# Performance work log

Hardware: AMD Instinct MI355X
Metric: run time of the kernel (lower is better)

## Reference

```python
import jax, jax.numpy as jnp
import numpy as np

N = 8192
F_IN = 128
F_OUT = 64
ALPHA = 0.2
NEG_INF = -9.0e15  # matches -9000000000000000.0 in the torch source


def setup_inputs() -> dict:
    key = jax.random.key(0)
    k1, k2, k3, k4 = jax.random.split(key, 4)
    h = jax.random.normal(k1, (N, F_IN), dtype=jnp.float32)
    adj = jax.random.randint(k2, (N, N), 0, 2).astype(jnp.int32)
    W = jax.random.normal(k3, (F_IN, F_OUT), dtype=jnp.float32) * 0.05
    a = jax.random.normal(k4, (2 * F_OUT,), dtype=jnp.float32) * 0.05
    return {"h": h, "adj": adj, "W": W, "a": a}


def reference(h, adj, W, a):
    # Wh: [N, F_OUT]
    Wh = h @ W
    # a([Wh_i ; Wh_j]) == Wh_i @ a1 + Wh_j @ a2 -> avoid O(N^2*2F) concat
    a1, a2 = a[:F_OUT], a[F_OUT:]
    s_src = Wh @ a1  # [N] contribution of row node i
    s_dst = Wh @ a2  # [N] contribution of col node j
    e = jax.nn.leaky_relu(s_src[:, None] + s_dst[None, :], negative_slope=ALPHA)  # [N, N]
    e = jnp.where(adj > 0, e, NEG_INF)
    attention = jax.nn.softmax(e, axis=1)  # [N, N]
    h_prime = attention @ Wh  # [N, F_OUT]
    return jax.nn.elu(h_prime)
```

## Files before the change

### kernel.cpp

```cpp
#include <hip/hip_runtime.h>
#include <hip/hip_bf16.h>

#define N 8192
#define FIN 128
#define FOUT 64
#define CSPLIT 2
#define CHUNK (N / CSPLIT)
#define M 32
#define TILE 128
#define NT (CHUNK / TILE)
#define LOG2E 1.44269504f

typedef __attribute__((ext_vector_type(4))) float f32x4;
typedef __attribute__((ext_vector_type(4))) int i32x4;
typedef __attribute__((ext_vector_type(8))) short bf16x8;

#define GLOAD_LDS16(gp, lp)                                                    \
    __builtin_amdgcn_global_load_lds(                                          \
        (const __attribute__((address_space(1))) void*)(gp),                   \
        (__attribute__((address_space(3))) void*)(lp), 16, 0, 0)

__global__ __launch_bounds__(256) void wh_kernel(
    const float* __restrict__ h, const float* __restrict__ W,
    const float* __restrict__ a,
    __hip_bfloat16* __restrict__ whT, float* __restrict__ s_src,
    float* __restrict__ s_dst) {
    __shared__ float Wl[FIN * FOUT];
    const int w = threadIdx.x >> 6;
    const int lane = threadIdx.x & 63;
#pragma unroll
    for (int q = 0; q < 8; ++q) {
        const int i = w * 8 + q;
        GLOAD_LDS16(W + i * 256 + lane * 4, &Wl[i * 256]);
    }
    asm volatile("s_waitcnt vmcnt(0)" ::: "memory");
    __syncthreads();

    const int row = blockIdx.x * 4 + w;
    const float* hr = h + (size_t)row * FIN;
    float acc = 0.f;
#pragma unroll
    for (int k0 = 0; k0 < FIN; k0 += 4) {
        f32x4 hv = *(const f32x4*)(hr + k0);
        acc += hv[0] * Wl[(k0 + 0) * FOUT + lane];
        acc += hv[1] * Wl[(k0 + 1) * FOUT + lane];
        acc += hv[2] * Wl[(k0 + 2) * FOUT + lane];
        acc += hv[3] * Wl[(k0 + 3) * FOUT + lane];
    }
    whT[(size_t)lane * N + row] = __float2bfloat16(acc);
    float s1 = acc * a[lane];
    float s2 = acc * a[FOUT + lane];
#pragma unroll
    for (int mm = 32; mm >= 1; mm >>= 1) {
        s1 += __shfl_xor(s1, mm, 64);
        s2 += __shfl_xor(s2, mm, 64);
    }
    if (lane == 0) { s_src[row] = s1 * LOG2E; s_dst[row] = s2 * LOG2E; }
}

__global__ __launch_bounds__(512, 4) void gat_partial(
    const int* __restrict__ adj, const __hip_bfloat16* __restrict__ whT,
    const float* __restrict__ s_src, const float* __restrict__ s_dst,
    float* __restrict__ numP, float* __restrict__ denP) {
    union SMem {
        struct {
            int adjb[2][M][TILE];
            short whb[2][FOUT][TILE];
            float sdl[CHUNK];
        } s;
        struct { float pC[4][M][FOUT]; float pD[4][M]; } e;
    };
    __shared__ SMem sm;

    const int tid = threadIdx.x;
    const int w = tid >> 6, lane = tid & 63;
    const int m = lane & 15, kg = lane >> 4;
    const int wr = w >> 2, wc = w & 3;
    const int rg = blockIdx.x >> 1;
    const int c = blockIdx.x & 1;
    const int ibase = rg * M;
    const int cb = c * CHUNK;
    const int aRow = wr * 16 + m;
    const float ssrc = s_src[ibase + aRow];
    const int sidx = w * 2;

    f32x4 acc[4] = {{0,0,0,0},{0,0,0,0},{0,0,0,0},{0,0,0,0}};
    f32x4 acc4 = {0,0,0,0};
    const short oneb = (m == 0) ? (short)0x3F80 : (short)0;
    const bf16x8 bones = {oneb, oneb, oneb, oneb, oneb, oneb, oneb, oneb};

    auto stage = [&](int t, int buf) {
        const int gcol = cb + t * TILE;
#pragma unroll
        for (int q = 0; q < 2; ++q) {
            const int idx = sidx + q;
            const int r = idx * 2 + (lane >> 5);
            const int b = ((lane & 31) * 16) ^ ((r & 31) << 4);
            GLOAD_LDS16(adj + (size_t)(ibase + r) * N + gcol + (b >> 2),
                        &sm.s.adjb[buf][idx * 2][0]);
        }
#pragma unroll
        for (int q = 0; q < 2; ++q) {
            const int idx = sidx + q;
            const int f = idx * 4 + (lane >> 4);
            const int b = ((lane & 15) * 16) ^ ((f & 15) << 4);
            GLOAD_LDS16(whT + (size_t)f * N + gcol + (b >> 1),
                        &sm.s.whb[buf][idx * 4][0]);
        }
    };

#pragma unroll
    for (int q = 0; q < 2; ++q) {
        const int idx = sidx + q;
        GLOAD_LDS16(s_dst + cb + idx * 256 + lane * 4, &sm.s.sdl[idx * 256]);
    }
    stage(0, 0);
    stage(1, 1);
    asm volatile("s_waitcnt vmcnt(4)" ::: "memory");
    __builtin_amdgcn_s_barrier();

#pragma unroll 2
    for (int t = 0; t < NT; ++t) {
        const int buf = t & 1;

        {
            const int kcol = wc * 32 + kg * 8;
            const char* adjbase = (const char*)&sm.s.adjb[buf][0][0];
            const int aswz = (aRow & 31) << 4;
            i32x4 a0 = *(const i32x4*)(adjbase + aRow * 512 + ((kcol * 4) ^ aswz));
            i32x4 a1 = *(const i32x4*)(adjbase + aRow * 512 + ((kcol * 4 + 16) ^ aswz));
            f32x4 d0 = *(const f32x4*)&sm.s.sdl[t * TILE + kcol];
            f32x4 d1 = *(const f32x4*)&sm.s.sdl[t * TILE + kcol + 4];
            const char* whbase = (const char*)&sm.s.whb[buf][0][0];
            bf16x8 bq0 = *(const bf16x8*)(whbase + (0 * 16 + m) * 256 + ((kcol * 2) ^ (m << 4)));
            bf16x8 bq1 = *(const bf16x8*)(whbase + (1 * 16 + m) * 256 + ((kcol * 2) ^ (m << 4)));
            bf16x8 bq2 = *(const bf16x8*)(whbase + (2 * 16 + m) * 256 + ((kcol * 2) ^ (m << 4)));
            bf16x8 bq3 = *(const bf16x8*)(whbase + (3 * 16 + m) * 256 + ((kcol * 2) ^ (m << 4)));

            float p[8];
#pragma unroll
            for (int e = 0; e < 4; ++e) {
                float x = ssrc + d0[e];
                float xl = fmaxf(x, 0.2f * x);
                float pe;
                asm("v_exp_f32 %0, %1" : "=v"(pe) : "v"(xl));
                p[e] = (a0[e] != 0) ? pe : 0.f;
            }
#pragma unroll
            for (int e = 0; e < 4; ++e) {
                float x = ssrc + d1[e];
                float xl = fmaxf(x, 0.2f * x);
                float pe;
                asm("v_exp_f32 %0, %1" : "=v"(pe) : "v"(xl));
                p[4 + e] = (a1[e] != 0) ? pe : 0.f;
            }
            union { bf16x8 v; unsigned u[4]; } afr;
#pragma unroll
            for (int q = 0; q < 4; ++q) {
                asm("v_cvt_pk_bf16_f32 %0, %1, %2"
                    : "=v"(afr.u[q]) : "v"(p[2 * q]), "v"(p[2 * q + 1]));
            }

            acc[0] = __builtin_amdgcn_mfma_f32_16x16x32_bf16(afr.v, bq0, acc[0], 0, 0, 0);
            acc[1] = __builtin_amdgcn_mfma_f32_16x16x32_bf16(afr.v, bq1, acc[1], 0, 0, 0);
            acc[2] = __builtin_amdgcn_mfma_f32_16x16x32_bf16(afr.v, bq2, acc[2], 0, 0, 0);
            acc[3] = __builtin_amdgcn_mfma_f32_16x16x32_bf16(afr.v, bq3, acc[3], 0, 0, 0);
            acc4   = __builtin_amdgcn_mfma_f32_16x16x32_bf16(afr.v, bones, acc4, 0, 0, 0);
        }

        __builtin_amdgcn_s_barrier();
        if (t + 2 < NT) {
            stage(t + 2, buf);
            asm volatile("s_waitcnt vmcnt(4)" ::: "memory");
            __builtin_amdgcn_s_barrier();
        } else if (t + 1 < NT) {
            asm volatile("s_waitcnt vmcnt(0)" ::: "memory");
            __builtin_amdgcn_s_barrier();
        }
    }

#pragma unroll
    for (int r = 0; r < 4; ++r) {
#pragma unroll
        for (int q = 0; q < 4; ++q) {
            sm.e.pC[wc][wr * 16 + kg * 4 + r][q * 16 + m] = acc[q][r];
        }
    }
    if (m == 0) {
#pragma unroll
        for (int r = 0; r < 4; ++r) {
            sm.e.pD[wc][wr * 16 + kg * 4 + r] = acc4[r];
        }
    }
    __syncthreads();

    float* numC = numP + (size_t)c * N * FOUT;
    float* denC = denP + (size_t)c * N;
#pragma unroll
    for (int k = 0; k < 4; ++k) {
        int idx = k * 512 + tid;
        int i = idx >> 6, f = idx & 63;
        float num = sm.e.pC[0][i][f] + sm.e.pC[1][i][f] + sm.e.pC[2][i][f] + sm.e.pC[3][i][f];
        numC[(size_t)(ibase + i) * FOUT + f] = num;
        if (f == 0) {
            denC[ibase + i] = sm.e.pD[0][i] + sm.e.pD[1][i] + sm.e.pD[2][i] + sm.e.pD[3][i];
        }
    }
}

__global__ __launch_bounds__(256) void gat_combine(
    const float* __restrict__ numP, const float* __restrict__ denP,
    float* __restrict__ out) {
    int idx = blockIdx.x * 256 + threadIdx.x;
    int row = idx >> 6;
    float num = 0.f, den = 0.f;
#pragma unroll
    for (int cc = 0; cc < CSPLIT; ++cc) {
        num += numP[(size_t)cc * N * FOUT + idx];
        den += denP[(size_t)cc * N + row];
    }
    float v = num / den;
    out[idx] = (v > 0.f) ? v : expm1f(v);
}

extern "C" void kernel_launch(void* const* d_in, const int* in_sizes, int n_in,
                              void* d_out, int out_size, void* d_ws, size_t ws_size,
                              hipStream_t stream) {
    const float* h = (const float*)d_in[0];
    const int* adj = (const int*)d_in[1];
    const float* W = (const float*)d_in[2];
    const float* a = (const float*)d_in[3];
    float* out = (float*)d_out;

    char* ws = (char*)d_ws;
    __hip_bfloat16* whT = (__hip_bfloat16*)ws;
    float* s_src = (float*)(ws + (size_t)FOUT * N * sizeof(__hip_bfloat16));
    float* s_dst = s_src + N;
    float* numP = s_dst + N;
    float* denP = numP + (size_t)CSPLIT * N * FOUT;

    hipLaunchKernelGGL(wh_kernel, dim3(N / 4), dim3(256), 0, stream,
                       h, W, a, whT, s_src, s_dst);
    hipLaunchKernelGGL(gat_partial, dim3((N / M) * CSPLIT), dim3(512), 0, stream,
                       adj, whT, s_src, s_dst, numP, denP);
    hipLaunchKernelGGL(gat_combine, dim3(N * FOUT / 256), dim3(256), 0, stream,
                       numP, denP, out);
}
```

Measured before the change: 80.67 us.

## Load Wh fragments directly to registers and triple-buffer adjacency tiles in LDS

The attention kernel no longer stages the transposed Wh tile through LDS. Each wave loads its bf16 B-fragments straight from global memory into registers with inline-asm loads, two tiles ahead, while the adjacency tiles move to a three-deep LDS ring with explicit vmcnt waits. This cuts LDS traffic and the associated bank work in the main loop, at the cost of more registers and fragile hand-counted waitcnts. Separately, the Wh projection kernel now computes four rows per wave, reusing each LDS W value across rows, and launches a quarter as many blocks.

```diff
diff --git a/kernel.cpp b/kernel.cpp
--- a/kernel.cpp
+++ b/kernel.cpp
@@ -36,26 +36,32 @@
     asm volatile("s_waitcnt vmcnt(0)" ::: "memory");
     __syncthreads();
 
-    const int row = blockIdx.x * 4 + w;
-    const float* hr = h + (size_t)row * FIN;
-    float acc = 0.f;
-#pragma unroll
+    const int rbase = blockIdx.x * 16 + w * 4;
+    float acc[4] = {0.f, 0.f, 0.f, 0.f};
     for (int k0 = 0; k0 < FIN; k0 += 4) {
-        f32x4 hv = *(const f32x4*)(hr + k0);
-        acc += hv[0] * Wl[(k0 + 0) * FOUT + lane];
-        acc += hv[1] * Wl[(k0 + 1) * FOUT + lane];
-        acc += hv[2] * Wl[(k0 + 2) * FOUT + lane];
-        acc += hv[3] * Wl[(k0 + 3) * FOUT + lane];
-    }
-    whT[(size_t)lane * N + row] = __float2bfloat16(acc);
-    float s1 = acc * a[lane];
-    float s2 = acc * a[FOUT + lane];
-#pragma unroll
-    for (int mm = 32; mm >= 1; mm >>= 1) {
-        s1 += __shfl_xor(s1, mm, 64);
-        s2 += __shfl_xor(s2, mm, 64);
-    }
-    if (lane == 0) { s_src[row] = s1 * LOG2E; s_dst[row] = s2 * LOG2E; }
+        float wv0 = Wl[(k0 + 0) * FOUT + lane];
+        float wv1 = Wl[(k0 + 1) * FOUT + lane];
+        float wv2 = Wl[(k0 + 2) * FOUT + lane];
+        float wv3 = Wl[(k0 + 3) * FOUT + lane];
+#pragma unroll
+        for (int rr = 0; rr < 4; ++rr) {
+            f32x4 hv = *(const f32x4*)(h + (size_t)(rbase + rr) * FIN + k0);
+            acc[rr] += hv[0] * wv0 + hv[1] * wv1 + hv[2] * wv2 + hv[3] * wv3;
+        }
+    }
+#pragma unroll
+    for (int rr = 0; rr < 4; ++rr) {
+        const int row = rbase + rr;
+        whT[(size_t)lane * N + row] = __float2bfloat16(acc[rr]);
+        float s1 = acc[rr] * a[lane];
+        float s2 = acc[rr] * a[FOUT + lane];
+#pragma unroll
+        for (int mm = 32; mm >= 1; mm >>= 1) {
+            s1 += __shfl_xor(s1, mm, 64);
+            s2 += __shfl_xor(s2, mm, 64);
+        }
+        if (lane == 0) { s_src[row] = s1 * LOG2E; s_dst[row] = s2 * LOG2E; }
+    }
 }
 
 __global__ __launch_bounds__(512, 4) void gat_partial(
@@ -64,8 +70,7 @@
     float* __restrict__ numP, float* __restrict__ denP) {
     union SMem {
         struct {
-            int adjb[2][M][TILE];
-            short whb[2][FOUT][TILE];
+            int adjb[3][M][TILE];
             float sdl[CHUNK];
         } s;
         struct { float pC[4][M][FOUT]; float pD[4][M]; } e;
@@ -83,101 +88,108 @@
     const int aRow = wr * 16 + m;
     const float ssrc = s_src[ibase + aRow];
     const int sidx = w * 2;
+    const int bcol = wc * 32 + kg * 8;
 
     f32x4 acc[4] = {{0,0,0,0},{0,0,0,0},{0,0,0,0},{0,0,0,0}};
     f32x4 acc4 = {0,0,0,0};
     const short oneb = (m == 0) ? (short)0x3F80 : (short)0;
     const bf16x8 bones = {oneb, oneb, oneb, oneb, oneb, oneb, oneb, oneb};
 
-    auto stage = [&](int t, int buf) {
-        const int gcol = cb + t * TILE;
-#pragma unroll
-        for (int q = 0; q < 2; ++q) {
-            const int idx = sidx + q;
-            const int r = idx * 2 + (lane >> 5);
-            const int b = ((lane & 31) * 16) ^ ((r & 31) << 4);
-            GLOAD_LDS16(adj + (size_t)(ibase + r) * N + gcol + (b >> 2),
-                        &sm.s.adjb[buf][idx * 2][0]);
-        }
-#pragma unroll
-        for (int q = 0; q < 2; ++q) {
-            const int idx = sidx + q;
-            const int f = idx * 4 + (lane >> 4);
-            const int b = ((lane & 15) * 16) ^ ((f & 15) << 4);
-            GLOAD_LDS16(whT + (size_t)f * N + gcol + (b >> 1),
-                        &sm.s.whb[buf][idx * 4][0]);
-        }
-    };
+    bf16x8 rb0_0, rb0_1, rb0_2, rb0_3;
+    bf16x8 rb1_0, rb1_1, rb1_2, rb1_3;
+
+#define STGA(T) do {                                                           \
+    const int gcol_ = cb + (T) * TILE;                                         \
+    _Pragma("unroll") for (int q_ = 0; q_ < 2; ++q_) {                         \
+        const int idx_ = sidx + q_;                                            \
+        const int r_ = idx_ * 2 + (lane >> 5);                                 \
+        const int b_ = ((lane & 31) * 16) ^ ((r_ & 31) << 4);                  \
+        GLOAD_LDS16(adj + (size_t)(ibase + r_) * N + gcol_ + (b_ >> 2),        \
+                    &sm.s.adjb[(T) % 3][idx_ * 2][0]);                         \
+    } } while (0)
+
+#define LDB(S, T) do {                                                         \
+    asm volatile("global_load_dwordx4 %0, %1, off" : "=v"(rb##S##_0)           \
+        : "v"(whT + (size_t)(0 * 16 + m) * N + cb + (T) * TILE + bcol));       \
+    asm volatile("global_load_dwordx4 %0, %1, off" : "=v"(rb##S##_1)           \
+        : "v"(whT + (size_t)(1 * 16 + m) * N + cb + (T) * TILE + bcol));       \
+    asm volatile("global_load_dwordx4 %0, %1, off" : "=v"(rb##S##_2)           \
+        : "v"(whT + (size_t)(2 * 16 + m) * N + cb + (T) * TILE + bcol));       \
+    asm volatile("global_load_dwordx4 %0, %1, off" : "=v"(rb##S##_3)           \
+        : "v"(whT + (size_t)(3 * 16 + m) * N + cb + (T) * TILE + bcol));       \
+    } while (0)
+
+#define WAITB(CNT, NS)                                                         \
+    asm volatile("s_waitcnt vmcnt(" CNT ")"                                    \
+        : "+v"(rb##NS##_0), "+v"(rb##NS##_1), "+v"(rb##NS##_2),                \
+          "+v"(rb##NS##_3) :: "memory");                                       \
+    __builtin_amdgcn_sched_barrier(0)
 
 #pragma unroll
     for (int q = 0; q < 2; ++q) {
         const int idx = sidx + q;
         GLOAD_LDS16(s_dst + cb + idx * 256 + lane * 4, &sm.s.sdl[idx * 256]);
     }
-    stage(0, 0);
-    stage(1, 1);
-    asm volatile("s_waitcnt vmcnt(4)" ::: "memory");
+    STGA(0); LDB(0, 0); STGA(1); LDB(1, 1); STGA(2);
+    WAITB("8", 0);
     __builtin_amdgcn_s_barrier();
 
-#pragma unroll 2
-    for (int t = 0; t < NT; ++t) {
-        const int buf = t & 1;
-
-        {
-            const int kcol = wc * 32 + kg * 8;
-            const char* adjbase = (const char*)&sm.s.adjb[buf][0][0];
-            const int aswz = (aRow & 31) << 4;
-            i32x4 a0 = *(const i32x4*)(adjbase + aRow * 512 + ((kcol * 4) ^ aswz));
-            i32x4 a1 = *(const i32x4*)(adjbase + aRow * 512 + ((kcol * 4 + 16) ^ aswz));
-            f32x4 d0 = *(const f32x4*)&sm.s.sdl[t * TILE + kcol];
-            f32x4 d1 = *(const f32x4*)&sm.s.sdl[t * TILE + kcol + 4];
-            const char* whbase = (const char*)&sm.s.whb[buf][0][0];
-            bf16x8 bq0 = *(const bf16x8*)(whbase + (0 * 16 + m) * 256 + ((kcol * 2) ^ (m << 4)));
-            bf16x8 bq1 = *(const bf16x8*)(whbase + (1 * 16 + m) * 256 + ((kcol * 2) ^ (m << 4)));
-            bf16x8 bq2 = *(const bf16x8*)(whbase + (2 * 16 + m) * 256 + ((kcol * 2) ^ (m << 4)));
-            bf16x8 bq3 = *(const bf16x8*)(whbase + (3 * 16 + m) * 256 + ((kcol * 2) ^ (m << 4)));
-
-            float p[8];
-#pragma unroll
-            for (int e = 0; e < 4; ++e) {
-                float x = ssrc + d0[e];
-                float xl = fmaxf(x, 0.2f * x);
-                float pe;
-                asm("v_exp_f32 %0, %1" : "=v"(pe) : "v"(xl));
-                p[e] = (a0[e] != 0) ? pe : 0.f;
-            }
-#pragma unroll
-            for (int e = 0; e < 4; ++e) {
-                float x = ssrc + d1[e];
-                float xl = fmaxf(x, 0.2f * x);
-                float pe;
-                asm("v_exp_f32 %0, %1" : "=v"(pe) : "v"(xl));
-                p[4 + e] = (a1[e] != 0) ? pe : 0.f;
-            }
-            union { bf16x8 v; unsigned u[4]; } afr;
-#pragma unroll
-            for (int q = 0; q < 4; ++q) {
-                asm("v_cvt_pk_bf16_f32 %0, %1, %2"
-                    : "=v"(afr.u[q]) : "v"(p[2 * q]), "v"(p[2 * q + 1]));
-            }
-
-            acc[0] = __builtin_amdgcn_mfma_f32_16x16x32_bf16(afr.v, bq0, acc[0], 0, 0, 0);
-            acc[1] = __builtin_amdgcn_mfma_f32_16x16x32_bf16(afr.v, bq1, acc[1], 0, 0, 0);
-            acc[2] = __builtin_amdgcn_mfma_f32_16x16x32_bf16(afr.v, bq2, acc[2], 0, 0, 0);
-            acc[3] = __builtin_amdgcn_mfma_f32_16x16x32_bf16(afr.v, bq3, acc[3], 0, 0, 0);
-            acc4   = __builtin_amdgcn_mfma_f32_16x16x32_bf16(afr.v, bones, acc4, 0, 0, 0);
-        }
-
-        __builtin_amdgcn_s_barrier();
-        if (t + 2 < NT) {
-            stage(t + 2, buf);
-            asm volatile("s_waitcnt vmcnt(4)" ::: "memory");
-            __builtin_amdgcn_s_barrier();
-        } else if (t + 1 < NT) {
-            asm volatile("s_waitcnt vmcnt(0)" ::: "memory");
-            __builtin_amdgcn_s_barrier();
-        }
-    }
+#define BODY(T, S, NS) do {                                                    \
+    const int t_ = (T);                                                        \
+    {                                                                          \
+        const char* adjbase = ((const char*)sm.s.adjb) + (t_ % 3) * (M * TILE * 4); \
+        const int aswz = (aRow & 31) << 4;                                     \
+        const int kcol = bcol;                                                 \
+        i32x4 a0 = *(const i32x4*)(adjbase + aRow * 512 + ((kcol * 4) ^ aswz)); \
+        i32x4 a1 = *(const i32x4*)(adjbase + aRow * 512 + ((kcol * 4 + 16) ^ aswz)); \
+        f32x4 d0 = *(const f32x4*)&sm.s.sdl[t_ * TILE + kcol];                 \
+        f32x4 d1 = *(const f32x4*)&sm.s.sdl[t_ * TILE + kcol + 4];             \
+        float p[8];                                                            \
+        _Pragma("unroll") for (int e = 0; e < 4; ++e) {                        \
+            float x = ssrc + d0[e];                                            \
+            float xl = fmaxf(x, 0.2f * x);                                     \
+            float pe;                                                          \
+            asm("v_exp_f32 %0, %1" : "=v"(pe) : "v"(xl));                      \
+            p[e] = (a0[e] != 0) ? pe : 0.f;                                    \
+        }                                                                      \
+        _Pragma("unroll") for (int e = 0; e < 4; ++e) {                        \
+            float x = ssrc + d1[e];                                            \
+            float xl = fmaxf(x, 0.2f * x);                                     \
+            float pe;                                                          \
+            asm("v_exp_f32 %0, %1" : "=v"(pe) : "v"(xl));                      \
+            p[4 + e] = (a1[e] != 0) ? pe : 0.f;                                \
+        }                                                                      \
+        union { bf16x8 v; unsigned u[4]; } afr;                                \
+        _Pragma("unroll") for (int q_ = 0; q_ < 4; ++q_) {                     \
+            asm("v_cvt_pk_bf16_f32 %0, %1, %2"                                 \
+                : "=v"(afr.u[q_]) : "v"(p[2 * q_]), "v"(p[2 * q_ + 1]));       \
+        }                                                                      \
+        acc[0] = __builtin_amdgcn_mfma_f32_16x16x32_bf16(afr.v, rb##S##_0, acc[0], 0, 0, 0); \
+        acc[1] = __builtin_amdgcn_mfma_f32_16x16x32_bf16(afr.v, rb##S##_1, acc[1], 0, 0, 0); \
+        acc[2] = __builtin_amdgcn_mfma_f32_16x16x32_bf16(afr.v, rb##S##_2, acc[2], 0, 0, 0); \
+        acc[3] = __builtin_amdgcn_mfma_f32_16x16x32_bf16(afr.v, rb##S##_3, acc[3], 0, 0, 0); \
+        acc4   = __builtin_amdgcn_mfma_f32_16x16x32_bf16(afr.v, bones, acc4, 0, 0, 0); \
+    }                                                                          \
+    __builtin_amdgcn_s_barrier();                                              \
+    if (t_ + 2 < NT) LDB(S, t_ + 2);                                           \
+    if (t_ + 3 < NT) STGA(t_ + 3);                                             \
+    if (t_ + 3 < NT)      { WAITB("8", NS); }                                  \
+    else if (t_ + 2 < NT) { WAITB("6", NS); }                                  \
+    else if (t_ + 1 < NT) { WAITB("0", NS); }                                  \
+    if (t_ + 1 < NT) __builtin_amdgcn_s_barrier();                             \
+    } while (0)
+
+    for (int tt = 0; tt < NT; tt += 2) {
+        BODY(tt, 0, 1);
+        BODY(tt + 1, 1, 0);
+    }
+
+#undef BODY
+#undef WAITB
+#undef LDB
+#undef STGA
+
+    __syncthreads();
 
 #pragma unroll
     for (int r = 0; r < 4; ++r) {
@@ -239,7 +251,7 @@
     float* numP = s_dst + N;
     float* denP = numP + (size_t)CSPLIT * N * FOUT;
 
-    hipLaunchKernelGGL(wh_kernel, dim3(N / 4), dim3(256), 0, stream,
+    hipLaunchKernelGGL(wh_kernel, dim3(N / 16), dim3(256), 0, stream,
                        h, W, a, whT, s_src, s_dst);
     hipLaunchKernelGGL(gat_partial, dim3((N / M) * CSPLIT), dim3(512), 0, stream,
                        adj, whT, s_src, s_dst, numP, denP);
```

Result: slower. 113.3 us (+40.4%).
